# Kernel tuning notes

Hardware: AMD Instinct MI355X
Metric: run time of the kernel (lower is better)

## Reference

```python
import jax, jax.numpy as jnp
import numpy as np

N_EMBD = 768
N_HEAD = 8
HEAD_DIM = N_EMBD // N_HEAD


def setup_inputs() -> dict:
    key = jax.random.key(0)
    k1, k2, k3 = jax.random.split(key, 3)
    B, T, C = 8, 1024, N_EMBD
    x = jax.random.normal(k1, (B, T, C), dtype=jnp.float32)
    # nn.Linear(C, 3C, bias=False): store as [C, 3C] so y = x @ W
    W_attn = jax.random.normal(k2, (C, 3 * C), dtype=jnp.float32) * (1.0 / np.sqrt(C))
    W_proj = jax.random.normal(k3, (C, C), dtype=jnp.float32) * (1.0 / np.sqrt(C))
    return {"x": x, "W_attn": W_attn, "W_proj": W_proj}


def reference(x, W_attn, W_proj):
    B, T, C = x.shape
    qkv = x @ W_attn                      # [B,T,3C]
    q, k, v = jnp.split(qkv, 3, axis=2)
    # [B,T,C] -> [B,H,T,D]
    def heads(t):
        return t.reshape(B, T, N_HEAD, HEAD_DIM).transpose(0, 2, 1, 3)
    q, k, v = heads(q), heads(k), heads(v)
    scale = 1.0 / np.sqrt(HEAD_DIM)
    att = jnp.einsum('bhtd,bhsd->bhts', q, k) * scale  # [B,H,T,T]
    causal = jnp.tril(jnp.ones((T, T), dtype=bool))
    att = jnp.where(causal[None, None], att, -jnp.inf)
    att = jax.nn.softmax(att, axis=-1)
    y = jnp.einsum('bhts,bhsd->bhtd', att, v)          # [B,H,T,D]
    y = y.transpose(0, 2, 1, 3).reshape(B, T, C)
    return y @ W_proj
```

## Files before the change

### kernel.cpp

```cpp
#include <hip/hip_runtime.h>
#include <stdint.h>

#define Bz 8
#define Tz 1024
#define Cz 768
#define Hz 8
#define Dz 96
#define BHz 64
#define Kz 768

typedef __bf16 bf16x8 __attribute__((ext_vector_type(8)));
typedef unsigned short u16x8 __attribute__((ext_vector_type(8)));
typedef float f32x4 __attribute__((ext_vector_type(4)));

__device__ __forceinline__ unsigned short f2bf(float f) {
  union { float f; unsigned int u; } v; v.f = f;
  unsigned int u = v.u;
  return (unsigned short)((u + 0x7fffu + ((u >> 16) & 1u)) >> 16);
}

typedef const __attribute__((address_space(1))) void* gas_ptr;
typedef __attribute__((address_space(3))) void* las_ptr;
__device__ __forceinline__ void gl16(const void* g, void* l) {
  __builtin_amdgcn_global_load_lds((gas_ptr)g, (las_ptr)l, 16, 0, 0);
}

__global__ __launch_bounds__(256) void cast_f32_bf16(const float* __restrict__ in,
                                                     unsigned short* __restrict__ out) {
  int i = (blockIdx.x * 256 + threadIdx.x) * 4;
  float4 v = *(const float4*)(in + i);
  union { unsigned short s[4]; uint2 u; } o;
  o.s[0] = f2bf(v.x); o.s[1] = f2bf(v.y); o.s[2] = f2bf(v.z); o.s[3] = f2bf(v.w);
  *(uint2*)(out + i) = o.u;
}

__global__ __launch_bounds__(256) void transpose_cast(const float* __restrict__ in,
                                                      unsigned short* __restrict__ out,
                                                      int R, int Cc) {
  __shared__ unsigned short t[64][72];
  int bx = blockIdx.x * 64;
  int by = blockIdx.y * 64;
  int tid = threadIdx.x;
#pragma unroll
  for (int i = 0; i < 16; i++) {
    int idx = tid + i * 256;
    int r = idx >> 6, c = idx & 63;
    t[c][r] = f2bf(in[(by + r) * Cc + bx + c]);
  }
  __syncthreads();
#pragma unroll
  for (int i = 0; i < 16; i++) {
    int idx = tid + i * 256;
    int r = idx >> 6, c = idx & 63;
    out[(bx + r) * R + by + c] = t[r][c];
  }
}

template <int MODE>
__global__ __launch_bounds__(256)
void gemm128(const unsigned short* __restrict__ A,
             const unsigned short* __restrict__ Bt,
             unsigned short* __restrict__ obf,
             float* __restrict__ of32) {
  __shared__ unsigned short Asm[128 * 32];
  __shared__ unsigned short Bsm[128 * 32];
  const int tid = threadIdx.x;
  const int wave = tid >> 6, lane = tid & 63;
  const int quad = lane >> 4, l16 = lane & 15;
  const int bm = blockIdx.x, bn = blockIdx.y;
  const int wm = (wave >> 1) * 64, wn = (wave & 1) * 64;

  f32x4 zero = {0.f, 0.f, 0.f, 0.f};
  f32x4 acc[4][4];
#pragma unroll
  for (int i = 0; i < 4; i++)
#pragma unroll
    for (int j = 0; j < 4; j++) acc[i][j] = zero;

  const int rr = lane >> 2, c8 = (lane & 3) * 8;
  const unsigned short* Ag0 = A + (size_t)(bm * 128 + wave * 32 + rr) * Kz + c8;
  const unsigned short* Ag1 = Ag0 + 16 * Kz;
  const unsigned short* Bg0 = Bt + (size_t)(bn * 128 + wave * 32 + rr) * Kz + c8;
  const unsigned short* Bg1 = Bg0 + 16 * Kz;
  unsigned short* lA0 = &Asm[wave * 1024];
  unsigned short* lA1 = lA0 + 512;
  unsigned short* lB0 = &Bsm[wave * 1024];
  unsigned short* lB1 = lB0 + 512;

  for (int k0 = 0; k0 < Kz; k0 += 32) {
    __syncthreads();
    gl16(Ag0 + k0, lA0);
    gl16(Ag1 + k0, lA1);
    gl16(Bg0 + k0, lB0);
    gl16(Bg1 + k0, lB1);
    __syncthreads();
    bf16x8 af[4], bfr[4];
#pragma unroll
    for (int mi = 0; mi < 4; mi++)
      af[mi] = *(const bf16x8*)&Asm[(wm + mi * 16 + l16) * 32 + quad * 8];
#pragma unroll
    for (int ni = 0; ni < 4; ni++)
      bfr[ni] = *(const bf16x8*)&Bsm[(wn + ni * 16 + l16) * 32 + quad * 8];
#pragma unroll
    for (int mi = 0; mi < 4; mi++)
#pragma unroll
      for (int ni = 0; ni < 4; ni++)
        acc[mi][ni] = __builtin_amdgcn_mfma_f32_16x16x32_bf16(af[mi], bfr[ni], acc[mi][ni], 0, 0, 0);
  }

#pragma unroll
  for (int mi = 0; mi < 4; mi++) {
    int row = bm * 128 + wm + mi * 16 + quad * 4;
    if (MODE == 0) {
      int b = row >> 10;
      int t = row & 1023;
#pragma unroll
      for (int ni = 0; ni < 4; ni++) {
        int col = bn * 128 + wn + ni * 16 + l16;
        int which = col / 768;
        int cc = col - which * 768;
        int h = cc / 96;
        int d = cc - h * 96;
        int base = ((which * 64 + b * 8 + h) * 1024 + t) * 96 + d;
#pragma unroll
        for (int r = 0; r < 4; r++) obf[base + r * 96] = f2bf(acc[mi][ni][r]);
      }
    } else {
#pragma unroll
      for (int ni = 0; ni < 4; ni++) {
        int col = bn * 128 + wn + ni * 16 + l16;
#pragma unroll
        for (int r = 0; r < 4; r++) of32[(row + r) * 768 + col] = acc[mi][ni][r];
      }
    }
  }
}

__global__ __launch_bounds__(256, 2)
void attn(const unsigned short* __restrict__ qkv, unsigned short* __restrict__ y) {
  const int bh = blockIdx.x;
  const int q0 = (7 - blockIdx.y) * 128;
  const int tid = threadIdx.x;
  const int wave = tid >> 6, lane = tid & 63;
  const int quad = lane >> 4, l16 = lane & 15;
  const int qw0 = q0 + wave * 32;
  const int b = bh >> 3, h = bh & 7;

  const unsigned short* Qh = qkv + bh * Tz * Dz;
  const unsigned short* Kh = qkv + (BHz + bh) * Tz * Dz;
  const unsigned short* Vh = qkv + (2 * BHz + bh) * Tz * Dz;

  __shared__ unsigned short Vsm[96 * 136];
  __shared__ unsigned short Psm[4 * 32 * 136];
  unsigned short* Pw = Psm + wave * 32 * 136;

  bf16x8 aq[2][3];
#pragma unroll
  for (int mi = 0; mi < 2; mi++)
#pragma unroll
    for (int kd = 0; kd < 3; kd++)
      aq[mi][kd] = *(const bf16x8*)(Qh + (qw0 + mi * 16 + l16) * Dz + kd * 32 + quad * 8);

  f32x4 zero = {0.f, 0.f, 0.f, 0.f};
  f32x4 acc_o[2][6];
#pragma unroll
  for (int mi = 0; mi < 2; mi++)
#pragma unroll
    for (int i = 0; i < 6; i++) acc_o[mi][i] = zero;
  const float NEG = -__builtin_inff();
  float mrow[2][4], lrow[2][4];
#pragma unroll
  for (int mi = 0; mi < 2; mi++)
#pragma unroll
    for (int r = 0; r < 4; r++) { mrow[mi][r] = NEG; lrow[mi][r] = 0.f; }
  const float scale = 0.10206207261596577f;

  const int sg = tid & 127;
  const int g0 = tid >> 7;
  const unsigned short* Vrow = Vh + sg * Dz;

  for (int s0 = 0; s0 <= q0; s0 += 128) {
    __syncthreads();
#pragma unroll
    for (int i = 0; i < 6; i++) {
      int g = g0 + 2 * i;
      u16x8 v = *(const u16x8*)(Vrow + s0 * Dz + g * 8);
#pragma unroll
      for (int jj = 0; jj < 8; jj++) Vsm[(g * 8 + jj) * 136 + sg] = v[jj];
    }
    __syncthreads();

    const int srem = qw0 + 31 - s0;
    const int nlim = min(7, srem >> 4);
    const int klim = min(3, srem >> 5);

    f32x4 sacc[2][8];
#pragma unroll
    for (int ni = 0; ni < 8; ni++) {
      if (ni <= nlim) {
        sacc[0][ni] = zero; sacc[1][ni] = zero;
#pragma unroll
        for (int kd = 0; kd < 3; kd++) {
          bf16x8 bk = *(const bf16x8*)(Kh + (s0 + ni * 16 + l16) * Dz + kd * 32 + quad * 8);
          sacc[0][ni] = __builtin_amdgcn_mfma_f32_16x16x32_bf16(aq[0][kd], bk, sacc[0][ni], 0, 0, 0);
          sacc[1][ni] = __builtin_amdgcn_mfma_f32_16x16x32_bf16(aq[1][kd], bk, sacc[1][ni], 0, 0, 0);
        }
      }
    }

#pragma unroll
    for (int mi = 0; mi < 2; mi++) {
      float rmax[4] = {NEG, NEG, NEG, NEG};
#pragma unroll
      for (int ni = 0; ni < 8; ni++) {
        if (ni <= nlim) {
#pragma unroll
          for (int r = 0; r < 4; r++) {
            int t_abs = qw0 + mi * 16 + quad * 4 + r;
            int s_abs = s0 + ni * 16 + l16;
            float v = (s_abs > t_abs) ? NEG : sacc[mi][ni][r] * scale;
            sacc[mi][ni][r] = v;
            rmax[r] = fmaxf(rmax[r], v);
          }
        }
      }
#pragma unroll
      for (int r = 0; r < 4; r++)
#pragma unroll
        for (int sh = 1; sh < 16; sh <<= 1)
          rmax[r] = fmaxf(rmax[r], __shfl_xor(rmax[r], sh));

      float alpha[4], rsum[4];
#pragma unroll
      for (int r = 0; r < 4; r++) {
        float mnew = fmaxf(mrow[mi][r], rmax[r]);
        alpha[r] = __expf(mrow[mi][r] - mnew);
        mrow[mi][r] = mnew;
        rsum[r] = 0.f;
      }
#pragma unroll
      for (int ni = 0; ni < 8; ni++) {
        if (ni <= nlim) {
#pragma unroll
          for (int r = 0; r < 4; r++) {
            float p = __expf(sacc[mi][ni][r] - mrow[mi][r]);
            rsum[r] += p;
            Pw[(mi * 16 + quad * 4 + r) * 136 + ni * 16 + l16] = f2bf(p);
          }
        }
      }
#pragma unroll
      for (int r = 0; r < 4; r++) {
#pragma unroll
        for (int sh = 1; sh < 16; sh <<= 1) rsum[r] += __shfl_xor(rsum[r], sh);
        lrow[mi][r] = lrow[mi][r] * alpha[r] + rsum[r];
      }
#pragma unroll
      for (int di = 0; di < 6; di++)
#pragma unroll
        for (int r = 0; r < 4; r++) acc_o[mi][di][r] *= alpha[r];
    }

#pragma unroll
    for (int kc = 0; kc < 4; kc++) {
      if (kc <= klim) {
        bf16x8 ap0 = *(const bf16x8*)&Pw[l16 * 136 + kc * 32 + quad * 8];
        bf16x8 ap1 = *(const bf16x8*)&Pw[(16 + l16) * 136 + kc * 32 + quad * 8];
#pragma unroll
        for (int di = 0; di < 6; di++) {
          bf16x8 bv = *(const bf16x8*)&Vsm[(di * 16 + l16) * 136 + kc * 32 + quad * 8];
          acc_o[0][di] = __builtin_amdgcn_mfma_f32_16x16x32_bf16(ap0, bv, acc_o[0][di], 0, 0, 0);
          acc_o[1][di] = __builtin_amdgcn_mfma_f32_16x16x32_bf16(ap1, bv, acc_o[1][di], 0, 0, 0);
        }
      }
    }
  }

#pragma unroll
  for (int mi = 0; mi < 2; mi++) {
#pragma unroll
    for (int r = 0; r < 4; r++) {
      float linv = 1.f / lrow[mi][r];
      int t = qw0 + mi * 16 + quad * 4 + r;
#pragma unroll
      for (int di = 0; di < 6; di++) {
        int d = di * 16 + l16;
        y[(b * Tz + t) * Cz + h * Dz + d] = f2bf(acc_o[mi][di][r] * linv);
      }
    }
  }
}

#define OFF_XB   0u
#define OFF_WAT  12582912u
#define OFF_WPT  16121856u
#define OFF_QKV  17301504u
#define OFF_Y    55050240u

extern "C" void kernel_launch(void* const* d_in, const int* in_sizes, int n_in,
                              void* d_out, int out_size, void* d_ws, size_t ws_size,
                              hipStream_t stream) {
  const float* x  = (const float*)d_in[0];
  const float* Wa = (const float*)d_in[1];
  const float* Wp = (const float*)d_in[2];
  float* out = (float*)d_out;
  uint8_t* ws = (uint8_t*)d_ws;
  unsigned short* xb  = (unsigned short*)(ws + OFF_XB);
  unsigned short* Wat = (unsigned short*)(ws + OFF_WAT);
  unsigned short* Wpt = (unsigned short*)(ws + OFF_WPT);
  unsigned short* qkv = (unsigned short*)(ws + OFF_QKV);
  unsigned short* y   = (unsigned short*)(ws + OFF_Y);

  cast_f32_bf16<<<6144, 256, 0, stream>>>(x, xb);
  transpose_cast<<<dim3(36, 12), 256, 0, stream>>>(Wa, Wat, 768, 2304);
  transpose_cast<<<dim3(12, 12), 256, 0, stream>>>(Wp, Wpt, 768, 768);
  gemm128<0><<<dim3(64, 18), 256, 0, stream>>>(xb, Wat, qkv, nullptr);
  attn<<<dim3(64, 8), 256, 0, stream>>>(qkv, y);
  gemm128<1><<<dim3(64, 6), 256, 0, stream>>>(y, Wpt, nullptr, out);
}
```

Measured before the change: 215.4 us.

## Store V transposed from QKV GEMM and streamline attention softmax

The QKV GEMM epilogue now writes V in a transposed [D,T] layout, so the attention kernel reads V fragments straight from global memory. This removes the per-tile shared-memory transpose and both block-wide barriers. The softmax switches to exp2 with the scale folded into one FMA. It only applies causal masking on diagonal tiles, skips the rescale when the running max grows by no more than a threshold (lazy rescaling), and defers the row-sum shuffle reduction to the end. The query-block order is also changed to interleave heavy and light tiles. The risks are uncoalesced global V loads in place of LDS reuse across the four waves, and a change in numerics from the lazy rescale.

```diff
diff --git a/kernel.cpp b/kernel.cpp
--- a/kernel.cpp
+++ b/kernel.cpp
@@ -18,6 +18,15 @@
   unsigned int u = v.u;
   return (unsigned short)((u + 0x7fffu + ((u >> 16) & 1u)) >> 16);
 }
+
+#if defined(__has_builtin)
+#if __has_builtin(__builtin_amdgcn_exp2f)
+#define EXP2(x) __builtin_amdgcn_exp2f(x)
+#endif
+#endif
+#ifndef EXP2
+#define EXP2(x) __expf((x) * 0.6931471805599453f)
+#endif
 
 typedef const __attribute__((address_space(1))) void* gas_ptr;
 typedef __attribute__((address_space(3))) void* las_ptr;
@@ -121,9 +130,17 @@
         int cc = col - which * 768;
         int h = cc / 96;
         int d = cc - h * 96;
-        int base = ((which * 64 + b * 8 + h) * 1024 + t) * 96 + d;
-#pragma unroll
-        for (int r = 0; r < 4; r++) obf[base + r * 96] = f2bf(acc[mi][ni][r]);
+        if (which == 2) {
+          int base = ((2 * 64 + b * 8 + h) * 96 + d) * 1024 + t;
+          union { unsigned short s[4]; uint2 u; } o;
+#pragma unroll
+          for (int r = 0; r < 4; r++) o.s[r] = f2bf(acc[mi][ni][r]);
+          *(uint2*)(obf + base) = o.u;
+        } else {
+          int base = ((which * 64 + b * 8 + h) * 1024 + t) * 96 + d;
+#pragma unroll
+          for (int r = 0; r < 4; r++) obf[base + r * 96] = f2bf(acc[mi][ni][r]);
+        }
       }
     } else {
 #pragma unroll
@@ -139,7 +156,8 @@
 __global__ __launch_bounds__(256, 2)
 void attn(const unsigned short* __restrict__ qkv, unsigned short* __restrict__ y) {
   const int bh = blockIdx.x;
-  const int q0 = (7 - blockIdx.y) * 128;
+  const int by = blockIdx.y;
+  const int q0 = ((by < 4) ? (7 - by) : (by - 4)) * 128;
   const int tid = threadIdx.x;
   const int wave = tid >> 6, lane = tid & 63;
   const int quad = lane >> 4, l16 = lane & 15;
@@ -148,9 +166,8 @@
 
   const unsigned short* Qh = qkv + bh * Tz * Dz;
   const unsigned short* Kh = qkv + (BHz + bh) * Tz * Dz;
-  const unsigned short* Vh = qkv + (2 * BHz + bh) * Tz * Dz;
-
-  __shared__ unsigned short Vsm[96 * 136];
+  const unsigned short* Vt = qkv + 2 * BHz * Tz * Dz + bh * Dz * Tz;
+
   __shared__ unsigned short Psm[4 * 32 * 136];
   unsigned short* Pw = Psm + wave * 32 * 136;
 
@@ -173,23 +190,9 @@
   for (int mi = 0; mi < 2; mi++)
 #pragma unroll
     for (int r = 0; r < 4; r++) { mrow[mi][r] = NEG; lrow[mi][r] = 0.f; }
-  const float scale = 0.10206207261596577f;
-
-  const int sg = tid & 127;
-  const int g0 = tid >> 7;
-  const unsigned short* Vrow = Vh + sg * Dz;
+  const float cs = 0.14724538519872735f;
 
   for (int s0 = 0; s0 <= q0; s0 += 128) {
-    __syncthreads();
-#pragma unroll
-    for (int i = 0; i < 6; i++) {
-      int g = g0 + 2 * i;
-      u16x8 v = *(const u16x8*)(Vrow + s0 * Dz + g * 8);
-#pragma unroll
-      for (int jj = 0; jj < 8; jj++) Vsm[(g * 8 + jj) * 136 + sg] = v[jj];
-    }
-    __syncthreads();
-
     const int srem = qw0 + 31 - s0;
     const int nlim = min(7, srem >> 4);
     const int klim = min(3, srem >> 5);
@@ -214,14 +217,15 @@
 #pragma unroll
       for (int ni = 0; ni < 8; ni++) {
         if (ni <= nlim) {
-#pragma unroll
-          for (int r = 0; r < 4; r++) {
-            int t_abs = qw0 + mi * 16 + quad * 4 + r;
-            int s_abs = s0 + ni * 16 + l16;
-            float v = (s_abs > t_abs) ? NEG : sacc[mi][ni][r] * scale;
-            sacc[mi][ni][r] = v;
-            rmax[r] = fmaxf(rmax[r], v);
+          if (s0 + ni * 16 + 15 > qw0 + mi * 16) {
+            const int t_base = qw0 + mi * 16 + quad * 4;
+            const int s_abs = s0 + ni * 16 + l16;
+#pragma unroll
+            for (int r = 0; r < 4; r++)
+              if (s_abs > t_base + r) sacc[mi][ni][r] = NEG;
           }
+#pragma unroll
+          for (int r = 0; r < 4; r++) rmax[r] = fmaxf(rmax[r], sacc[mi][ni][r]);
         }
       }
 #pragma unroll
@@ -230,35 +234,38 @@
         for (int sh = 1; sh < 16; sh <<= 1)
           rmax[r] = fmaxf(rmax[r], __shfl_xor(rmax[r], sh));
 
-      float alpha[4], rsum[4];
-#pragma unroll
-      for (int r = 0; r < 4; r++) {
-        float mnew = fmaxf(mrow[mi][r], rmax[r]);
-        alpha[r] = __expf(mrow[mi][r] - mnew);
-        mrow[mi][r] = mnew;
-        rsum[r] = 0.f;
-      }
+      int ok = 1;
+#pragma unroll
+      for (int r = 0; r < 4; r++) ok &= (rmax[r] <= mrow[mi][r] + 54.0f) ? 1 : 0;
+      if (!__all(ok)) {
+#pragma unroll
+        for (int r = 0; r < 4; r++) {
+          float mnew = fmaxf(mrow[mi][r], rmax[r]);
+          float alpha = EXP2((mrow[mi][r] - mnew) * cs);
+          mrow[mi][r] = mnew;
+          lrow[mi][r] *= alpha;
+#pragma unroll
+          for (int di = 0; di < 6; di++) acc_o[mi][di][r] *= alpha;
+        }
+      }
+
+      float nmc[4];
+#pragma unroll
+      for (int r = 0; r < 4; r++) nmc[r] = -mrow[mi][r] * cs;
+      float rsum[4] = {0.f, 0.f, 0.f, 0.f};
 #pragma unroll
       for (int ni = 0; ni < 8; ni++) {
         if (ni <= nlim) {
 #pragma unroll
           for (int r = 0; r < 4; r++) {
-            float p = __expf(sacc[mi][ni][r] - mrow[mi][r]);
+            float p = EXP2(fmaf(sacc[mi][ni][r], cs, nmc[r]));
             rsum[r] += p;
             Pw[(mi * 16 + quad * 4 + r) * 136 + ni * 16 + l16] = f2bf(p);
           }
         }
       }
 #pragma unroll
-      for (int r = 0; r < 4; r++) {
-#pragma unroll
-        for (int sh = 1; sh < 16; sh <<= 1) rsum[r] += __shfl_xor(rsum[r], sh);
-        lrow[mi][r] = lrow[mi][r] * alpha[r] + rsum[r];
-      }
-#pragma unroll
-      for (int di = 0; di < 6; di++)
-#pragma unroll
-        for (int r = 0; r < 4; r++) acc_o[mi][di][r] *= alpha[r];
+      for (int r = 0; r < 4; r++) lrow[mi][r] += rsum[r];
     }
 
 #pragma unroll
@@ -268,7 +275,7 @@
         bf16x8 ap1 = *(const bf16x8*)&Pw[(16 + l16) * 136 + kc * 32 + quad * 8];
 #pragma unroll
         for (int di = 0; di < 6; di++) {
-          bf16x8 bv = *(const bf16x8*)&Vsm[(di * 16 + l16) * 136 + kc * 32 + quad * 8];
+          bf16x8 bv = *(const bf16x8*)(Vt + (di * 16 + l16) * Tz + s0 + kc * 32 + quad * 8);
           acc_o[0][di] = __builtin_amdgcn_mfma_f32_16x16x32_bf16(ap0, bv, acc_o[0][di], 0, 0, 0);
           acc_o[1][di] = __builtin_amdgcn_mfma_f32_16x16x32_bf16(ap1, bv, acc_o[1][di], 0, 0, 0);
         }
@@ -280,6 +287,9 @@
   for (int mi = 0; mi < 2; mi++) {
 #pragma unroll
     for (int r = 0; r < 4; r++) {
+#pragma unroll
+      for (int sh = 1; sh < 16; sh <<= 1)
+        lrow[mi][r] += __shfl_xor(lrow[mi][r], sh);
       float linv = 1.f / lrow[mi][r];
       int t = qw0 + mi * 16 + quad * 4 + r;
 #pragma unroll
```

Result: slower. 223.5 us (+3.7%).
